# Kernel optimization log

Measured on AMD Instinct MI355X. Metric: run time of the kernel, lower is better.

The kernel has to match this reference:

```python
import jax, jax.numpy as jnp
import numpy as np

GROUPS = 32
EPS = 1e-5


def group_norm(x, w, b):
    B, C, H, W = x.shape
    xg = x.reshape(B, GROUPS, C // GROUPS, H, W)
    mu = xg.mean(axis=(2, 3, 4), keepdims=True)
    var = xg.var(axis=(2, 3, 4), keepdims=True)
    xn = ((xg - mu) / jnp.sqrt(var + EPS)).reshape(B, C, H, W)
    return xn * w[None, :, None, None] + b[None, :, None, None]


def setup_inputs() -> dict:
    key = jax.random.key(0)
    ks = jax.random.split(key, 4)
    B, C, H, W = 8, 512, 32, 32
    x = jax.random.normal(ks[0], (B, C, H, W), dtype=jnp.float32)
    gn_w = jnp.ones((C,), dtype=jnp.float32)
    gn_b = jnp.zeros((C,), dtype=jnp.float32)
    # 1x1 conv weights, scaled like typical init for numerical sanity
    qkv_w = jax.random.normal(ks[1], (3 * C, C), dtype=jnp.float32) * (1.0 / np.sqrt(C))
    proj_w = jax.random.normal(ks[2], (C, C), dtype=jnp.float32) * (1.0 / np.sqrt(C))
    proj_b = jnp.zeros((C,), dtype=jnp.float32)
    return {"x": x, "gn_w": gn_w, "gn_b": gn_b, "qkv_w": qkv_w,
            "proj_w": proj_w, "proj_b": proj_b, "num_heads": 8}


def reference(x, gn_w, gn_b, qkv_w, proj_w, proj_b, num_heads):
    B, C, H, W = x.shape
    N = H * W
    head_dim = C // num_heads
    xn = group_norm(x, gn_w, gn_b)
    # 1x1 conv == channel matmul: (B, 3C, N)
    qkv = jnp.einsum('oc,bcn->bon', qkv_w, xn.reshape(B, C, N))
    # faithful to torch: reshape to (B*nh, 3*hd, N) then chunk into thirds
    qkv = qkv.reshape(B * num_heads, 3 * head_dim, N)
    q, k, v = jnp.split(qkv, 3, axis=1)  # each (B*nh, hd, N)
    scale = 1.0 / np.sqrt(np.sqrt(head_dim))
    attn = jax.nn.softmax(jnp.einsum('bct,bcs->bts', q * scale, k * scale), axis=-1)
    h = jnp.einsum('bts,bcs->bct', attn, v)  # (B*nh, hd, N)
    h = h.reshape(B, C, N)
    out = jnp.einsum('oc,bcn->bon', proj_w, h) + proj_b[None, :, None]
    return out.reshape(B, C, H, W) + x
```

## Files before the change

### kernel.cpp

```cpp
#include <hip/hip_runtime.h>

#define B_ 8
#define C_ 512
#define N_ 1024
#define GROUPS_ 32
#define CPG_ 16
#define NH_ 8
#define HD_ 64

typedef _Float16 half8 __attribute__((ext_vector_type(8)));
typedef _Float16 half2v __attribute__((ext_vector_type(2)));
typedef float f32x4 __attribute__((ext_vector_type(4)));
typedef float f32x16 __attribute__((ext_vector_type(16)));

#define QSCALE 0.18033688011112042f
#define THR_LOG2 11.0f

__device__ __forceinline__ void gload_lds16(const void* g, void* l) {
  __builtin_amdgcn_global_load_lds(
      (const __attribute__((address_space(1))) unsigned int*)g,
      (__attribute__((address_space(3))) unsigned int*)l, 16, 0, 0);
}

__global__ __launch_bounds__(256) void prep(
    const float* __restrict__ qkv_w, const float* __restrict__ proj_w,
    const float* __restrict__ x, _Float16* __restrict__ qkw,
    _Float16* __restrict__ vw, _Float16* __restrict__ pw,
    float2* __restrict__ stats) {
  const int tid = threadIdx.x;
  if (blockIdx.x < 512) {
    const int R = blockIdx.x * 4 + (tid >> 6);
    const int k = (tid & 63) * 8;
    const float* src;
    _Float16* dst;
    float sc = 1.f;
    if (R < 1024) {
      const int head = R >> 7, r = R & 127;
      src = qkv_w + (size_t)(head * 192 + r) * 512;
      if (r < 64) sc = QSCALE;
      dst = qkw + (size_t)R * 512;
    } else if (R < 1536) {
      const int vr = R - 1024;
      const int head = vr >> 6, c = vr & 63;
      src = qkv_w + (size_t)(head * 192 + 128 + c) * 512;
      dst = vw + (size_t)vr * 512;
    } else {
      src = proj_w + (size_t)(R - 1536) * 512;
      dst = pw + (size_t)(R - 1536) * 512;
    }
    const float4 v0 = *reinterpret_cast<const float4*>(src + k);
    const float4 v1 = *reinterpret_cast<const float4*>(src + k + 4);
    _Float16 h[8] = {(_Float16)(v0.x * sc), (_Float16)(v0.y * sc),
                     (_Float16)(v0.z * sc), (_Float16)(v0.w * sc),
                     (_Float16)(v1.x * sc), (_Float16)(v1.y * sc),
                     (_Float16)(v1.z * sc), (_Float16)(v1.w * sc)};
    *reinterpret_cast<float4*>(dst + k) = *reinterpret_cast<float4*>(h);
  } else {
    const int bg = blockIdx.x - 512;
    const int b = bg / GROUPS_, g = bg % GROUPS_;
    const float* xp = x + ((size_t)b * C_ + (size_t)g * CPG_) * N_;
    const int total = CPG_ * N_;
    float s = 0.f, ss = 0.f;
    for (int i = tid * 4; i < total; i += 1024) {
      const float4 v = *reinterpret_cast<const float4*>(xp + i);
      s += v.x + v.y + v.z + v.w;
      ss += v.x * v.x + v.y * v.y + v.z * v.z + v.w * v.w;
    }
#pragma unroll
    for (int off = 32; off > 0; off >>= 1) {
      s += __shfl_down(s, off);
      ss += __shfl_down(ss, off);
    }
    __shared__ float red[8];
    if ((tid & 63) == 0) { red[tid >> 6] = s; red[4 + (tid >> 6)] = ss; }
    __syncthreads();
    if (tid == 0) {
      s = red[0] + red[1] + red[2] + red[3];
      ss = red[4] + red[5] + red[6] + red[7];
      const float inv = 1.0f / (float)total;
      const float mu = s * inv;
      const float var = ss * inv - mu * mu;
      stats[bg] = make_float2(mu, rsqrtf(var + 1e-5f));
    }
  }
}

__global__ __launch_bounds__(256) void gn_norm(const float* __restrict__ x,
                                               const float* __restrict__ gw,
                                               const float* __restrict__ gb,
                                               const float2* __restrict__ stats,
                                               _Float16* __restrict__ xnT) {
  const int n0 = blockIdx.x * 16;
  const int b = blockIdx.y;
  __shared__ _Float16 T[16][520];
  __shared__ float wsh[512], bsh[512];
  const int tid = threadIdx.x;
  for (int c = tid; c < 512; c += 256) {
    const float2 st = stats[b * 32 + (c >> 4)];
    const float wv = gw[c] * st.y;
    wsh[c] = wv;
    bsh[c] = gb[c] - st.x * wv;
  }
  __syncthreads();
  {
    const int n = tid & 15;
    const int cb = tid >> 4;
    const float* xb = x + (size_t)b * C_ * N_ + n0 + n;
#pragma unroll
    for (int i = 0; i < 32; ++i) {
      const int c = i * 16 + cb;
      T[n][c] = (_Float16)(xb[(size_t)c * N_] * wsh[c] + bsh[c]);
    }
  }
  __syncthreads();
  const int row = tid >> 4;
  const int seg = tid & 15;
  _Float16* dst = &xnT[((size_t)b * N_ + n0 + row) * C_ + seg * 32];
  const _Float16* srcp = &T[row][seg * 32];
  *reinterpret_cast<float4*>(dst) = *reinterpret_cast<const float4*>(srcp);
  *reinterpret_cast<float4*>(dst + 8) = *reinterpret_cast<const float4*>(srcp + 8);
  *reinterpret_cast<float4*>(dst + 16) = *reinterpret_cast<const float4*>(srcp + 16);
  *reinterpret_cast<float4*>(dst + 24) = *reinterpret_cast<const float4*>(srcp + 24);
}

template <bool OUT_HALF, bool EPI>
__global__ __launch_bounds__(256, 2) void gemm_tn(
    const _Float16* __restrict__ A, long strideAb,
    const _Float16* __restrict__ Bm, long strideBb,
    void* __restrict__ D, long strideDb, int ldd, int K,
    const float* __restrict__ bias, const float* __restrict__ resid,
    long strideRb) {
  const int bc0 = blockIdx.x * 128;
  const int ar0 = blockIdx.y * 128;
  const int b = blockIdx.z;
  const _Float16* Ab = A + (size_t)b * strideAb;
  const _Float16* Bb = Bm + (size_t)b * strideBb;

  __shared__ _Float16 As[2][128][64];
  __shared__ _Float16 Bs[2][128][64];

  const int tid = threadIdx.x;
  const int lane = tid & 63;
  const int wid = tid >> 6;
  const int war = (wid >> 1) * 64;
  const int wbc = (wid & 1) * 64;
  const int lg = lane >> 4;
  const int lr = lane & 15;

  const int srow = lane >> 3;
  const int sgr = (lane & 7) ^ srow;

#define STAGE(buf, koff)                                                     \
  _Pragma("unroll") for (int i = 0; i < 4; ++i) {                            \
    const int rb = (i * 4 + wid) * 8;                                        \
    gload_lds16(&Ab[(size_t)(ar0 + rb + srow) * K + (koff) + sgr * 8],       \
                &As[buf][rb][0]);                                            \
    gload_lds16(&Bb[(size_t)(bc0 + rb + srow) * K + (koff) + sgr * 8],       \
                &Bs[buf][rb][0]);                                            \
  }

  f32x4 acc[4][4] = {};

  STAGE(0, 0)
  __syncthreads();

  const int nsteps = K >> 6;
  int cur = 0;
  for (int step = 0; step < nsteps; ++step) {
    if (step + 1 < nsteps) { STAGE(cur ^ 1, (step + 1) << 6) }
    const half8* Ah = reinterpret_cast<const half8*>(&As[cur][0][0]);
    const half8* Bh = reinterpret_cast<const half8*>(&Bs[cur][0][0]);
#pragma unroll
    for (int kc = 0; kc < 2; ++kc) {
      half8 af[4], bf[4];
#pragma unroll
      for (int i = 0; i < 4; ++i)
        af[i] = Ah[(war + i * 16 + lr) * 8 + ((4 * kc + lg) ^ (lr & 7))];
#pragma unroll
      for (int j = 0; j < 4; ++j)
        bf[j] = Bh[(wbc + j * 16 + lr) * 8 + ((4 * kc + lg) ^ (lr & 7))];
#pragma unroll
      for (int i = 0; i < 4; ++i)
#pragma unroll
        for (int j = 0; j < 4; ++j)
          acc[i][j] = __builtin_amdgcn_mfma_f32_16x16x32_f16(af[i], bf[j],
                                                             acc[i][j], 0, 0, 0);
    }
    __syncthreads();
    cur ^= 1;
  }
#undef STAGE

  if (OUT_HALF) {
    _Float16* Dp = (_Float16*)D + (size_t)b * strideDb;
#pragma unroll
    for (int i = 0; i < 4; ++i)
#pragma unroll
      for (int r = 0; r < 4; ++r) {
        const int row = ar0 + war + i * 16 + lg * 4 + r;
#pragma unroll
        for (int j = 0; j < 4; ++j) {
          const int col = bc0 + wbc + j * 16 + lr;
          Dp[(size_t)row * ldd + col] = (_Float16)acc[i][j][r];
        }
      }
  }
  if (EPI) {
    float* Dp = (float*)D + (size_t)b * strideDb;
    const float* Rp = resid + (size_t)b * strideRb;
#pragma unroll
    for (int i = 0; i < 4; ++i)
#pragma unroll
      for (int r = 0; r < 4; ++r) {
        const int row = ar0 + war + i * 16 + lg * 4 + r;
        const float bv = bias[row];
#pragma unroll
        for (int j = 0; j < 4; ++j) {
          const int col = bc0 + wbc + j * 16 + lr;
          const size_t off = (size_t)row * ldd + col;
          Dp[off] = acc[i][j][r] + bv + Rp[off];
        }
      }
  }
}

__global__ __launch_bounds__(256, 2) void attn_mfma(
    const _Float16* __restrict__ qkT, const _Float16* __restrict__ vT,
    _Float16* __restrict__ hT) {
  const int qb = blockIdx.x * 128;
  const int bh = blockIdx.y;
  const int b = bh >> 3, head = bh & 7;
  const int tid = threadIdx.x;
  const int lane = tid & 63;
  const int w = tid >> 6;
  const int l31 = lane & 31;
  const int lg2 = lane >> 5;

  __shared__ _Float16 Ks[64][72];
  __shared__ _Float16 Vs[64][72];

  const size_t qkbase = (size_t)b * N_ * 1024;

  half8 bfq[4];
#pragma unroll
  for (int kc = 0; kc < 4; ++kc)
    bfq[kc] = *reinterpret_cast<const half8*>(
        &qkT[qkbase + (size_t)(qb + w * 32 + l31) * 1024 + head * 128 +
             kc * 16 + lg2 * 8]);

  const int sr = tid >> 2;
  const int sc = (tid & 3) * 16;
  const _Float16* kp0 = qkT + qkbase + (size_t)sr * 1024 + head * 128 + 64 + sc;
  const _Float16* vp0 = vT + ((size_t)bh * 64 + sr) * 1024 + sc;

  float4 kreg0 = *reinterpret_cast<const float4*>(kp0);
  float4 kreg1 = *reinterpret_cast<const float4*>(kp0 + 8);
  float4 vreg0 = *reinterpret_cast<const float4*>(vp0);
  float4 vreg1 = *reinterpret_cast<const float4*>(vp0 + 8);

  f32x16 oacc[2];
#pragma unroll
  for (int ct = 0; ct < 2; ++ct)
#pragma unroll
    for (int r = 0; r < 16; ++r) oacc[ct][r] = 0.f;
  float m_run = -1e30f, l_run = 0.f;

  for (int t = 0; t < 16; ++t) {
    __syncthreads();
    *reinterpret_cast<float4*>(&Ks[sr][sc]) = kreg0;
    *reinterpret_cast<float4*>(&Ks[sr][sc + 8]) = kreg1;
    *reinterpret_cast<float4*>(&Vs[sr][sc]) = vreg0;
    *reinterpret_cast<float4*>(&Vs[sr][sc + 8]) = vreg1;
    __syncthreads();
    {
      const int sbn = (t < 15) ? (t + 1) * 64 : 960;
      kreg0 = *reinterpret_cast<const float4*>(kp0 + (size_t)sbn * 1024);
      kreg1 = *reinterpret_cast<const float4*>(kp0 + (size_t)sbn * 1024 + 8);
      vreg0 = *reinterpret_cast<const float4*>(vp0 + sbn);
      vreg1 = *reinterpret_cast<const float4*>(vp0 + sbn + 8);
    }

    f32x16 sacc[2];
#pragma unroll
    for (int st = 0; st < 2; ++st)
#pragma unroll
      for (int r = 0; r < 16; ++r) sacc[st][r] = 0.f;
    __builtin_amdgcn_s_setprio(1);
#pragma unroll
    for (int st = 0; st < 2; ++st)
#pragma unroll
      for (int kc = 0; kc < 4; ++kc) {
        const half8 af = *reinterpret_cast<const half8*>(
            &Ks[st * 32 + l31][kc * 16 + lg2 * 8]);
        sacc[st] = __builtin_amdgcn_mfma_f32_32x32x16_f16(af, bfq[kc],
                                                          sacc[st], 0, 0, 0);
      }
    __builtin_amdgcn_s_setprio(0);

    float mt = -1e30f;
#pragma unroll
    for (int st = 0; st < 2; ++st)
#pragma unroll
      for (int r = 0; r < 16; ++r) mt = fmaxf(mt, sacc[st][r]);
    mt = fmaxf(mt, __shfl_xor(mt, 32));
    if (!__all(mt <= m_run + THR_LOG2)) {
      const float mn = fmaxf(m_run, mt);
      const float alpha = exp2f(m_run - mn);
      m_run = mn;
      l_run *= alpha;
#pragma unroll
      for (int r = 0; r < 16; ++r) {
        const int qrow = (r & 3) + 8 * (r >> 2) + 4 * lg2;
        const float ar = __shfl(alpha, qrow);
        oacc[0][r] *= ar;
        oacc[1][r] *= ar;
      }
    }
    const float mr = m_run;
    float ps = 0.f;
#pragma unroll
    for (int st = 0; st < 2; ++st)
#pragma unroll
      for (int r = 0; r < 16; ++r) {
        const float p = exp2f(sacc[st][r] - mr);
        sacc[st][r] = p;
        ps += p;
      }
    ps += __shfl_xor(ps, 32);
    l_run += ps;

    half8 pa[4];
    {
      unsigned int wo[2][8];
#pragma unroll
      for (int st = 0; st < 2; ++st)
#pragma unroll
        for (int m = 0; m < 8; ++m) {
          union { half2v h; unsigned int u; } cv;
          cv.h.x = (_Float16)sacc[st][2 * m];
          cv.h.y = (_Float16)sacc[st][2 * m + 1];
          wo[st][m] = cv.u;
        }
#pragma unroll
      for (int kc = 0; kc < 4; ++kc) {
        const int st = kc >> 1;
        const int base = 4 * (kc & 1);
        const unsigned int a0 = wo[st][base], a1 = wo[st][base + 1];
        const unsigned int a2 = wo[st][base + 2], a3 = wo[st][base + 3];
        const unsigned int x0 = __shfl_xor(a0, 32);
        const unsigned int x1 = __shfl_xor(a1, 32);
        const unsigned int x2 = __shfl_xor(a2, 32);
        const unsigned int x3 = __shfl_xor(a3, 32);
        union { unsigned int u[4]; half8 h; } fr;
        fr.u[0] = lg2 ? x2 : a0;
        fr.u[1] = lg2 ? x3 : a1;
        fr.u[2] = lg2 ? a2 : x0;
        fr.u[3] = lg2 ? a3 : x1;
        pa[kc] = fr.h;
      }
    }

    __builtin_amdgcn_s_setprio(1);
#pragma unroll
    for (int ct = 0; ct < 2; ++ct)
#pragma unroll
      for (int ks = 0; ks < 4; ++ks) {
        const half8 vf = *reinterpret_cast<const half8*>(
            &Vs[ct * 32 + l31][ks * 16 + lg2 * 8]);
        oacc[ct] = __builtin_amdgcn_mfma_f32_32x32x16_f16(pa[ks], vf,
                                                          oacc[ct], 0, 0, 0);
      }
    __builtin_amdgcn_s_setprio(0);
  }

  const size_t hbase = ((size_t)b * N_ + qb) * C_ + head * 64;
  const float linv = 1.f / l_run;
#pragma unroll
  for (int r = 0; r < 16; ++r) {
    const int qrow = (r & 3) + 8 * (r >> 2) + 4 * lg2;
    const float li = __shfl(linv, qrow);
    const size_t rowoff = hbase + (size_t)(w * 32 + qrow) * C_;
#pragma unroll
    for (int ct = 0; ct < 2; ++ct)
      hT[rowoff + ct * 32 + l31] = (_Float16)(oacc[ct][r] * li);
  }
}

extern "C" void kernel_launch(void* const* d_in, const int* in_sizes, int n_in,
                              void* d_out, int out_size, void* d_ws,
                              size_t ws_size, hipStream_t stream) {
  const float* x = (const float*)d_in[0];
  const float* gn_w = (const float*)d_in[1];
  const float* gn_b = (const float*)d_in[2];
  const float* qkv_w = (const float*)d_in[3];
  const float* proj_w = (const float*)d_in[4];
  const float* proj_b = (const float*)d_in[5];
  float* out = (float*)d_out;

  char* ws = (char*)d_ws;
  const size_t MB = 1024 * 1024;
  _Float16* qkw = (_Float16*)(ws);
  _Float16* vw = (_Float16*)(ws + 1 * MB);
  _Float16* pw = (_Float16*)(ws + 3 * MB / 2);
  float2* stats = (float2*)(ws + 2 * MB);
  _Float16* xnT = (_Float16*)(ws + 3 * MB);
  _Float16* qkT = (_Float16*)(ws + 11 * MB);
  _Float16* vT = (_Float16*)(ws + 27 * MB);
  _Float16* hT = (_Float16*)(ws + 35 * MB);

  prep<<<dim3(768), 256, 0, stream>>>(qkv_w, proj_w, x, qkw, vw, pw, stats);
  gn_norm<<<dim3(64, B_), 256, 0, stream>>>(x, gn_w, gn_b, stats, xnT);
  gemm_tn<true, false><<<dim3(8, 8, B_), 256, 0, stream>>>(
      xnT, (long)N_ * C_, qkw, 0L, qkT, (long)N_ * 1024, 1024, C_,
      nullptr, nullptr, 0L);
  gemm_tn<true, false><<<dim3(8, 4, B_), 256, 0, stream>>>(
      vw, 0L, xnT, (long)N_ * C_, vT, (long)512 * 1024, 1024, C_,
      nullptr, nullptr, 0L);
  attn_mfma<<<dim3(N_ / 128, B_ * NH_), 256, 0, stream>>>(qkT, vT, hT);
  gemm_tn<false, true><<<dim3(8, 4, B_), 256, 0, stream>>>(
      pw, 0L, hT, (long)N_ * C_, out, (long)C_ * N_, N_, C_,
      proj_b, x, (long)C_ * N_);
}
```

Baseline: 171.1 us.

## Merge QK and V GEMMs, narrow proj tiles, double-buffer attention K/V via LDS DMA

The separate QK and V projection GEMMs become one launch with a 12-row grid, where blocks pick their operands from blockIdx.y. The output projection now uses 128x64 tiles, doubling the block count to fill more CUs. The attention kernel drops its register-staged K/V copy and padded LDS for double-buffered direct global-to-LDS loads with an XOR swizzle, so the next tile's fetch overlaps compute and one barrier per iteration is removed. The cost is more LDS per attention block and smaller per-block reuse in the projection GEMM.

After: 168.8 us. No clear change (-1.4%).

```diff
diff --git a/kernel.cpp b/kernel.cpp
--- a/kernel.cpp
+++ b/kernel.cpp
@@ -123,18 +123,27 @@
   *reinterpret_cast<float4*>(dst + 24) = *reinterpret_cast<const float4*>(srcp + 24);
 }
 
-template <bool OUT_HALF, bool EPI>
-__global__ __launch_bounds__(256, 2) void gemm_tn(
-    const _Float16* __restrict__ A, long strideAb,
-    const _Float16* __restrict__ Bm, long strideBb,
-    void* __restrict__ D, long strideDb, int ldd, int K,
-    const float* __restrict__ bias, const float* __restrict__ resid,
-    long strideRb) {
+__global__ __launch_bounds__(256, 2) void gemm_qkv(
+    const _Float16* __restrict__ xnT, const _Float16* __restrict__ qkw,
+    const _Float16* __restrict__ vw, _Float16* __restrict__ qkT,
+    _Float16* __restrict__ vT) {
+  const int b = blockIdx.z;
   const int bc0 = blockIdx.x * 128;
-  const int ar0 = blockIdx.y * 128;
-  const int b = blockIdx.z;
-  const _Float16* Ab = A + (size_t)b * strideAb;
-  const _Float16* Bb = Bm + (size_t)b * strideBb;
+  int ar0;
+  const _Float16 *Ab, *Bb;
+  _Float16* Dp;
+  if (blockIdx.y < 8) {
+    ar0 = blockIdx.y * 128;
+    Ab = xnT + (size_t)b * N_ * C_;
+    Bb = qkw;
+    Dp = qkT + (size_t)b * N_ * 1024;
+  } else {
+    ar0 = (blockIdx.y - 8) * 128;
+    Ab = vw;
+    Bb = xnT + (size_t)b * N_ * C_;
+    Dp = vT + (size_t)b * 512 * 1024;
+  }
+  const int K = 512;
 
   __shared__ _Float16 As[2][128][64];
   __shared__ _Float16 Bs[2][128][64];
@@ -164,10 +173,10 @@
   STAGE(0, 0)
   __syncthreads();
 
-  const int nsteps = K >> 6;
   int cur = 0;
-  for (int step = 0; step < nsteps; ++step) {
-    if (step + 1 < nsteps) { STAGE(cur ^ 1, (step + 1) << 6) }
+#pragma unroll 1
+  for (int step = 0; step < 8; ++step) {
+    if (step + 1 < 8) { STAGE(cur ^ 1, (step + 1) << 6) }
     const half8* Ah = reinterpret_cast<const half8*>(&As[cur][0][0]);
     const half8* Bh = reinterpret_cast<const half8*>(&Bs[cur][0][0]);
 #pragma unroll
@@ -191,37 +200,102 @@
   }
 #undef STAGE
 
-  if (OUT_HALF) {
-    _Float16* Dp = (_Float16*)D + (size_t)b * strideDb;
-#pragma unroll
-    for (int i = 0; i < 4; ++i)
-#pragma unroll
-      for (int r = 0; r < 4; ++r) {
-        const int row = ar0 + war + i * 16 + lg * 4 + r;
-#pragma unroll
-        for (int j = 0; j < 4; ++j) {
-          const int col = bc0 + wbc + j * 16 + lr;
-          Dp[(size_t)row * ldd + col] = (_Float16)acc[i][j][r];
-        }
-      }
-  }
-  if (EPI) {
-    float* Dp = (float*)D + (size_t)b * strideDb;
-    const float* Rp = resid + (size_t)b * strideRb;
-#pragma unroll
-    for (int i = 0; i < 4; ++i)
-#pragma unroll
-      for (int r = 0; r < 4; ++r) {
-        const int row = ar0 + war + i * 16 + lg * 4 + r;
-        const float bv = bias[row];
-#pragma unroll
-        for (int j = 0; j < 4; ++j) {
-          const int col = bc0 + wbc + j * 16 + lr;
-          const size_t off = (size_t)row * ldd + col;
-          Dp[off] = acc[i][j][r] + bv + Rp[off];
-        }
-      }
-  }
+#pragma unroll
+  for (int i = 0; i < 4; ++i)
+#pragma unroll
+    for (int r = 0; r < 4; ++r) {
+      const int row = ar0 + war + i * 16 + lg * 4 + r;
+#pragma unroll
+      for (int j = 0; j < 4; ++j) {
+        const int col = bc0 + wbc + j * 16 + lr;
+        Dp[(size_t)row * 1024 + col] = (_Float16)acc[i][j][r];
+      }
+    }
+}
+
+__global__ __launch_bounds__(256, 2) void gemm_proj(
+    const _Float16* __restrict__ pw, const _Float16* __restrict__ hT,
+    float* __restrict__ out, const float* __restrict__ bias,
+    const float* __restrict__ resid) {
+  const int bc0 = blockIdx.x * 64;
+  const int ar0 = blockIdx.y * 128;
+  const int b = blockIdx.z;
+  const _Float16* Bb = hT + (size_t)b * N_ * C_;
+  const int K = 512;
+
+  __shared__ _Float16 As[2][128][64];
+  __shared__ _Float16 Bs[2][64][64];
+
+  const int tid = threadIdx.x;
+  const int lane = tid & 63;
+  const int wid = tid >> 6;
+  const int war = (wid >> 1) * 64;
+  const int wbc = (wid & 1) * 32;
+  const int lg = lane >> 4;
+  const int lr = lane & 15;
+
+  const int srow = lane >> 3;
+  const int sgr = (lane & 7) ^ srow;
+
+#define STAGEP(buf, koff)                                                    \
+  _Pragma("unroll") for (int i = 0; i < 4; ++i) {                            \
+    const int rb = (i * 4 + wid) * 8;                                        \
+    gload_lds16(&pw[(size_t)(ar0 + rb + srow) * K + (koff) + sgr * 8],       \
+                &As[buf][rb][0]);                                            \
+  }                                                                          \
+  _Pragma("unroll") for (int i = 0; i < 2; ++i) {                            \
+    const int rb = (i * 4 + wid) * 8;                                        \
+    gload_lds16(&Bb[(size_t)(bc0 + rb + srow) * K + (koff) + sgr * 8],       \
+                &Bs[buf][rb][0]);                                            \
+  }
+
+  f32x4 acc[4][2] = {};
+
+  STAGEP(0, 0)
+  __syncthreads();
+
+  int cur = 0;
+#pragma unroll 1
+  for (int step = 0; step < 8; ++step) {
+    if (step + 1 < 8) { STAGEP(cur ^ 1, (step + 1) << 6) }
+    const half8* Ah = reinterpret_cast<const half8*>(&As[cur][0][0]);
+    const half8* Bh = reinterpret_cast<const half8*>(&Bs[cur][0][0]);
+#pragma unroll
+    for (int kc = 0; kc < 2; ++kc) {
+      half8 af[4], bf[2];
+#pragma unroll
+      for (int i = 0; i < 4; ++i)
+        af[i] = Ah[(war + i * 16 + lr) * 8 + ((4 * kc + lg) ^ (lr & 7))];
+#pragma unroll
+      for (int j = 0; j < 2; ++j)
+        bf[j] = Bh[(wbc + j * 16 + lr) * 8 + ((4 * kc + lg) ^ (lr & 7))];
+#pragma unroll
+      for (int i = 0; i < 4; ++i)
+#pragma unroll
+        for (int j = 0; j < 2; ++j)
+          acc[i][j] = __builtin_amdgcn_mfma_f32_16x16x32_f16(af[i], bf[j],
+                                                             acc[i][j], 0, 0, 0);
+    }
+    __syncthreads();
+    cur ^= 1;
+  }
+#undef STAGEP
+
+  float* Dp = out + (size_t)b * C_ * N_;
+  const float* Rp = resid + (size_t)b * C_ * N_;
+#pragma unroll
+  for (int i = 0; i < 4; ++i)
+#pragma unroll
+    for (int r = 0; r < 4; ++r) {
+      const int row = ar0 + war + i * 16 + lg * 4 + r;
+      const float bv = bias[row];
+#pragma unroll
+      for (int j = 0; j < 2; ++j) {
+        const int col = bc0 + wbc + j * 16 + lr;
+        const size_t off = (size_t)row * N_ + col;
+        Dp[off] = acc[i][j][r] + bv + Rp[off];
+      }
+    }
 }
 
 __global__ __launch_bounds__(256, 2) void attn_mfma(
@@ -236,8 +310,8 @@
   const int l31 = lane & 31;
   const int lg2 = lane >> 5;
 
-  __shared__ _Float16 Ks[64][72];
-  __shared__ _Float16 Vs[64][72];
+  __shared__ _Float16 Ks[2][64][64];
+  __shared__ _Float16 Vs[2][64][64];
 
   const size_t qkbase = (size_t)b * N_ * 1024;
 
@@ -248,15 +322,17 @@
         &qkT[qkbase + (size_t)(qb + w * 32 + l31) * 1024 + head * 128 +
              kc * 16 + lg2 * 8]);
 
-  const int sr = tid >> 2;
-  const int sc = (tid & 3) * 16;
-  const _Float16* kp0 = qkT + qkbase + (size_t)sr * 1024 + head * 128 + 64 + sc;
-  const _Float16* vp0 = vT + ((size_t)bh * 64 + sr) * 1024 + sc;
-
-  float4 kreg0 = *reinterpret_cast<const float4*>(kp0);
-  float4 kreg1 = *reinterpret_cast<const float4*>(kp0 + 8);
-  float4 vreg0 = *reinterpret_cast<const float4*>(vp0);
-  float4 vreg1 = *reinterpret_cast<const float4*>(vp0 + 8);
+  const int srow = lane >> 3;
+  const int sgrh = ((lane & 7) ^ srow) * 8;
+  const int r0 = w * 16 + srow;
+  const _Float16* kp = qkT + qkbase + head * 128 + 64 + sgrh;
+  const _Float16* vp = vT + (size_t)bh * 64 * 1024 + sgrh;
+
+#define STAGEA(buf, sb)                                                      \
+  gload_lds16(kp + (size_t)((sb) + r0) * 1024, &Ks[buf][w * 16][0]);         \
+  gload_lds16(kp + (size_t)((sb) + r0 + 8) * 1024, &Ks[buf][w * 16 + 8][0]); \
+  gload_lds16(vp + (size_t)r0 * 1024 + (sb), &Vs[buf][w * 16][0]);           \
+  gload_lds16(vp + (size_t)(r0 + 8) * 1024 + (sb), &Vs[buf][w * 16 + 8][0]);
 
   f32x16 oacc[2];
 #pragma unroll
@@ -265,20 +341,13 @@
     for (int r = 0; r < 16; ++r) oacc[ct][r] = 0.f;
   float m_run = -1e30f, l_run = 0.f;
 
+  STAGEA(0, 0)
+  __syncthreads();
+
+  int cur = 0;
+#pragma unroll 1
   for (int t = 0; t < 16; ++t) {
-    __syncthreads();
-    *reinterpret_cast<float4*>(&Ks[sr][sc]) = kreg0;
-    *reinterpret_cast<float4*>(&Ks[sr][sc + 8]) = kreg1;
-    *reinterpret_cast<float4*>(&Vs[sr][sc]) = vreg0;
-    *reinterpret_cast<float4*>(&Vs[sr][sc + 8]) = vreg1;
-    __syncthreads();
-    {
-      const int sbn = (t < 15) ? (t + 1) * 64 : 960;
-      kreg0 = *reinterpret_cast<const float4*>(kp0 + (size_t)sbn * 1024);
-      kreg1 = *reinterpret_cast<const float4*>(kp0 + (size_t)sbn * 1024 + 8);
-      vreg0 = *reinterpret_cast<const float4*>(vp0 + sbn);
-      vreg1 = *reinterpret_cast<const float4*>(vp0 + sbn + 8);
-    }
+    if (t < 15) { STAGEA(cur ^ 1, (t + 1) * 64) }
 
     f32x16 sacc[2];
 #pragma unroll
@@ -291,7 +360,7 @@
 #pragma unroll
       for (int kc = 0; kc < 4; ++kc) {
         const half8 af = *reinterpret_cast<const half8*>(
-            &Ks[st * 32 + l31][kc * 16 + lg2 * 8]);
+            &Ks[cur][st * 32 + l31][((kc * 2 + lg2) ^ (l31 & 7)) * 8]);
         sacc[st] = __builtin_amdgcn_mfma_f32_32x32x16_f16(af, bfq[kc],
                                                           sacc[st], 0, 0, 0);
       }
@@ -366,12 +435,16 @@
 #pragma unroll
       for (int ks = 0; ks < 4; ++ks) {
         const half8 vf = *reinterpret_cast<const half8*>(
-            &Vs[ct * 32 + l31][ks * 16 + lg2 * 8]);
+            &Vs[cur][ct * 32 + l31][((ks * 2 + lg2) ^ (l31 & 7)) * 8]);
         oacc[ct] = __builtin_amdgcn_mfma_f32_32x32x16_f16(pa[ks], vf,
                                                           oacc[ct], 0, 0, 0);
       }
     __builtin_amdgcn_s_setprio(0);
-  }
+
+    __syncthreads();
+    cur ^= 1;
+  }
+#undef STAGEA
 
   const size_t hbase = ((size_t)b * N_ + qb) * C_ + head * 64;
   const float linv = 1.f / l_run;
@@ -410,14 +483,7 @@
 
   prep<<<dim3(768), 256, 0, stream>>>(qkv_w, proj_w, x, qkw, vw, pw, stats);
   gn_norm<<<dim3(64, B_), 256, 0, stream>>>(x, gn_w, gn_b, stats, xnT);
-  gemm_tn<true, false><<<dim3(8, 8, B_), 256, 0, stream>>>(
-      xnT, (long)N_ * C_, qkw, 0L, qkT, (long)N_ * 1024, 1024, C_,
-      nullptr, nullptr, 0L);
-  gemm_tn<true, false><<<dim3(8, 4, B_), 256, 0, stream>>>(
-      vw, 0L, xnT, (long)N_ * C_, vT, (long)512 * 1024, 1024, C_,
-      nullptr, nullptr, 0L);
+  gemm_qkv<<<dim3(8, 12, B_), 256, 0, stream>>>(xnT, qkw, vw, qkT, vT);
   attn_mfma<<<dim3(N_ / 128, B_ * NH_), 256, 0, stream>>>(qkT, vT, hT);
-  gemm_tn<false, true><<<dim3(8, 4, B_), 256, 0, stream>>>(
-      pw, 0L, hT, (long)N_ * C_, out, (long)C_ * N_, N_, C_,
-      proj_b, x, (long)C_ * N_);
-}
+  gemm_proj<<<dim3(16, 4, B_), 256, 0, stream>>>(pw, hT, out, proj_b, x);
+}
```
